# Performance work log

Measured on AMD Instinct MI355X. Metric: run time of the kernel, lower is better.

Reference implementation:

```python
import jax, jax.numpy as jnp
from jax import lax
import numpy as np

HIDDEN = 1024
FEAT = 512
PREV = 10
PRED = 20
BATCH = 1024


def setup_inputs() -> dict:
    key = jax.random.key(0)
    ks = jax.random.split(key, 12)
    s_in = 1.0 / np.sqrt(FEAT)
    s_h = 1.0 / np.sqrt(HIDDEN)
    return {
        "real_input": jax.random.normal(ks[0], (BATCH, PREV + PRED, FEAT), jnp.float32),
        "fake_input": jax.random.normal(ks[1], (BATCH, PRED, FEAT), jnp.float32),
        "Wx": jax.random.normal(ks[2], (FEAT, 4 * HIDDEN), jnp.float32) * s_in,
        "Wh": jax.random.normal(ks[3], (HIDDEN, 4 * HIDDEN), jnp.float32) * s_h,
        "b": jnp.zeros((4 * HIDDEN,), jnp.float32),
        "w2": jax.random.normal(ks[4], (HIDDEN, 1), jnp.float32) * s_h,
        "b2": jnp.zeros((1,), jnp.float32),
        "w3": jax.random.normal(ks[5], (1, 1), jnp.float32),
        "b3": jnp.zeros((1,), jnp.float32),
        "w4": jax.random.normal(ks[6], (1, 1), jnp.float32),
        "b4": jnp.zeros((1,), jnp.float32),
    }


def _lstm_hidden_states(seq, Wx, Wh, b):
    # seq: [B, T, F] -> hidden states hs: [T, B, H]
    B = seq.shape[0]
    xz = jnp.einsum("btf,fk->btk", seq, Wx) + b  # precompute input projections

    def step(carry, xz_t):
        h, c = carry
        z = xz_t + h @ Wh  # [B, 4H]
        i, f, g, o = jnp.split(z, 4, axis=-1)
        i = jax.nn.sigmoid(i)
        f = jax.nn.sigmoid(f)
        g = jnp.tanh(g)
        o = jax.nn.sigmoid(o)
        c = f * c + i * g
        h = o * jnp.tanh(c)
        return (h, c), h

    h0 = jnp.zeros((B, Wh.shape[0]), seq.dtype)
    _, hs = lax.scan(step, (h0, h0), jnp.swapaxes(xz, 0, 1))
    return hs


def _dense_chain(h, w2, b2, w3, b3, w4, b4):
    x = jnp.tanh(h @ w2 + b2)
    x = jnp.tanh(x @ w3 + b3)
    x = jnp.tanh(x @ w4 + b4)
    return x


def reference(real_input, fake_input, Wx, Wh, b, w2, b2, w3, b3, w4, b4):
    # trajectory_real[k] is the prefix real_input[:, :PREV+k+1]; running the
    # LSTM from zero state over each prefix equals taking hidden state at
    # step PREV+k of a single scan over the full sequence.
    fake_seq = jnp.concatenate([real_input[:, :PREV, :], fake_input], axis=1)

    hs_real = _lstm_hidden_states(real_input, Wx, Wh, b)[PREV:PREV + PRED]  # [PRED,B,H]
    hs_fake = _lstm_hidden_states(fake_seq, Wx, Wh, b)[PREV:PREV + PRED]

    real_pred = _dense_chain(hs_real, w2, b2, w3, b3, w4, b4)  # [PRED,B,1]
    fake_pred = _dense_chain(hs_fake, w2, b2, w3, b3, w4, b4)

    real_pred = jnp.swapaxes(real_pred, 0, 1)  # [B,PRED,1]
    fake_pred = jnp.swapaxes(fake_pred, 0, 1)
    return real_pred, fake_pred
```

## Files before the change

### kernel.cpp

```cpp
#include <hip/hip_runtime.h>
#include <hip/hip_bf16.h>
#include <stdint.h>
#include <string.h>

#define HIDDEN 1024
#define FEAT   512
#define PREV   10
#define PRED   20
#define BATCH  1024
#define KTOT   (HIDDEN + FEAT)
#define N4H    4096
#define TSTEPS (PREV + PRED)
#define NBLK   512
#define NTHR   512

typedef __attribute__((ext_vector_type(8))) short short8;
typedef __attribute__((ext_vector_type(4))) float f32x4;
typedef unsigned long long ull;

typedef __attribute__((address_space(3))) unsigned int u32_lds;
typedef const __attribute__((address_space(1))) unsigned int u32_gbl;

__device__ __forceinline__ void async16(void* lds, const void* g) {
  u32_lds* lp = (u32_lds*)(unsigned int)(uintptr_t)lds;
  u32_gbl* gp = (u32_gbl*)(uintptr_t)g;
  __builtin_amdgcn_global_load_lds(gp, lp, 16, 0, 0);
}

__device__ __forceinline__ float sigmoidf_(float x) {
  return 1.0f / (1.0f + __expf(-x));
}
__device__ __forceinline__ float tanhf_(float x) {
  return 1.0f - 2.0f / (1.0f + __expf(2.0f * x));
}

__device__ __forceinline__ ull cload(const void* p) {
  return __hip_atomic_load((const ull*)p, __ATOMIC_RELAXED, __HIP_MEMORY_SCOPE_AGENT);
}
__device__ __forceinline__ void cstore(void* p, ull v) {
  __hip_atomic_store((ull*)p, v, __ATOMIC_RELAXED, __HIP_MEMORY_SCOPE_AGENT);
}

__global__ void pack_w_kernel(const float* __restrict__ Wx, const float* __restrict__ Wh,
                              __hip_bfloat16* __restrict__ WpT) {
  __shared__ float tile[64][65];
  const int k0 = blockIdx.x * 64, n0 = blockIdx.y * 64;
  const int tid = threadIdx.x;
  const float* src = (k0 < HIDDEN) ? (Wh + (size_t)k0 * N4H) : (Wx + (size_t)(k0 - HIDDEN) * N4H);
  {
    const int jl = tid & 15, g = (tid >> 4) & 3, klb = tid >> 6;
#pragma unroll
    for (int it = 0; it < 16; ++it) {
      int kl = klb + it * 4;
      tile[kl][4 * jl + g] = src[(size_t)kl * N4H + g * HIDDEN + (n0 >> 2) + jl];
    }
  }
  __syncthreads();
  {
    const int kl = tid & 63, nlb = tid >> 6;
#pragma unroll
    for (int it = 0; it < 16; ++it) {
      int nl = nlb + it * 4;
      WpT[(size_t)(n0 + nl) * KTOT + k0 + kl] = __float2bfloat16(tile[kl][nl]);
    }
  }
}

__global__ void pack_bias_kernel(const float* __restrict__ b, float* __restrict__ bp) {
  int n = blockIdx.x * 256 + threadIdx.x;
  if (n < N4H) bp[n] = b[(n & 3) * HIDDEN + (n >> 2)];
}

__global__ void cvt_x_kernel(const float* __restrict__ xr, const float* __restrict__ xf,
                             __hip_bfloat16* __restrict__ xrb, __hip_bfloat16* __restrict__ xfb) {
  const int NR4 = BATCH * TSTEPS * FEAT / 4;
  const int NF4 = BATCH * PRED * FEAT / 4;
  int i = blockIdx.x * 256 + threadIdx.x;
  float4 v;
  __hip_bfloat16* dst;
  if (i < NR4) {
    v = ((const float4*)xr)[i];
    dst = xrb + (size_t)i * 4;
  } else {
    int j = i - NR4;
    if (j >= NF4) return;
    v = ((const float4*)xf)[j];
    dst = xfb + (size_t)j * 4;
  }
  dst[0] = __float2bfloat16(v.x);
  dst[1] = __float2bfloat16(v.y);
  dst[2] = __float2bfloat16(v.z);
  dst[3] = __float2bfloat16(v.w);
}

__global__ __launch_bounds__(512, 4)
void lstm_persistent(const __hip_bfloat16* __restrict__ xrb,
                     const __hip_bfloat16* __restrict__ xfb,
                     const __hip_bfloat16* __restrict__ WpT,
                     const float* __restrict__ biasp,
                     const float* __restrict__ w2,
                     __hip_bfloat16* __restrict__ hb0,
                     __hip_bfloat16* __restrict__ hb1,
                     float* __restrict__ cbuf,
                     float* __restrict__ accout,
                     unsigned* __restrict__ bar) {
  __shared__ __align__(16) char smem[40960];
  char* smA = smem;
  char* smB = smem + 8192;

  const int tid = threadIdx.x;
  const int bid = blockIdx.x;
  const int nt = bid & 15, rt = bid >> 4;
  const int n0 = nt * 256;
  const int r0 = rt * 64;
  const int w = tid >> 6, l = tid & 63;
  const int sub = l >> 3;
  const int csrc = (l & 7) ^ sub;
  const int quad = l >> 4, lrow = l & 15;
  const int wm = w & 1, wn = w >> 1;
  const int row_e = tid >> 3, jq = tid & 7;
  unsigned* cnt = bar;
  unsigned* flag = bar + 32;

  const unsigned short* wp_us = (const unsigned short*)WpT;
  float creg[8] = {0.f, 0.f, 0.f, 0.f, 0.f, 0.f, 0.f, 0.f};

#pragma unroll 1
  for (int t = 0; t < TSTEPS; ++t) {
    const unsigned short* hcur = (const unsigned short*)((t & 1) ? hb1 : hb0);
    unsigned short* hnext = (unsigned short*)((t & 1) ? hb0 : hb1);
    const bool active = (t >= PREV) || (rt < 16);

    if (active) {
      if (t == PREV && r0 >= BATCH) {
#pragma unroll
        for (int h2 = 0; h2 < 2; ++h2) {
          size_t base = (size_t)(r0 - BATCH + row_e) * HIDDEN + nt * 64 + h2 * 32 + jq * 4;
          ull d0 = cload(&cbuf[base]);
          ull d1 = cload(&cbuf[base + 2]);
          float2 f0 = *(float2*)&d0, f1 = *(float2*)&d1;
          creg[h2 * 4 + 0] = f0.x;
          creg[h2 * 4 + 1] = f0.y;
          creg[h2 * 4 + 2] = f1.x;
          creg[h2 * 4 + 3] = f1.y;
        }
      }
      const int r0h = (t == PREV && r0 >= BATCH) ? (r0 - BATCH) : r0;

      f32x4 acc[2][4];
#pragma unroll
      for (int a = 0; a < 2; ++a)
#pragma unroll
        for (int b_ = 0; b_ < 4; ++b_) acc[a][b_] = (f32x4){0.f, 0.f, 0.f, 0.f};

#pragma unroll 1
      for (int kt = 0; kt < KTOT / 64; ++kt) {
        const int k0 = kt * 64;
        const unsigned short* bb = wp_us + (size_t)n0 * KTOT + k0;
#pragma unroll
        for (int it = 0; it < 4; ++it)
          async16(smB + (w * 32 + it * 8) * 128,
                  bb + (size_t)(w * 32 + it * 8 + sub) * KTOT + csrc * 8);
        if (k0 < HIDDEN) {
          const unsigned short* ap = hcur + (size_t)(r0h + w * 8 + sub) * HIDDEN + k0 + csrc * 8;
          ull d0 = cload(ap);
          ull d1 = cload(ap + 4);
          ull* lw = (ull*)(smA + (w * 8 + sub) * 128 + (l & 7) * 16);
          lw[0] = d0;
          lw[1] = d1;
        } else {
          const unsigned short* xb;
          size_t xstr;
          if (r0 < BATCH) {
            xb = (const unsigned short*)xrb + ((size_t)r0 * TSTEPS + t) * FEAT + (k0 - HIDDEN);
            xstr = TSTEPS * FEAT;
          } else {
            xb = (const unsigned short*)xfb + ((size_t)(r0 - BATCH) * PRED + (t - PREV)) * FEAT + (k0 - HIDDEN);
            xstr = PRED * FEAT;
          }
          async16(smA + (w * 8) * 128, xb + (size_t)(w * 8 + sub) * xstr + csrc * 8);
        }
        __syncthreads();
#pragma unroll
        for (int kk = 0; kk < 2; ++kk) {
          const int swz = (((kk << 2) + quad) ^ (lrow & 7)) * 16;
          short8 af[2], bf[4];
#pragma unroll
          for (int mi = 0; mi < 2; ++mi)
            af[mi] = *(const short8*)(smA + (wm * 32 + mi * 16 + lrow) * 128 + swz);
#pragma unroll
          for (int ni = 0; ni < 4; ++ni)
            bf[ni] = *(const short8*)(smB + (wn * 64 + ni * 16 + lrow) * 128 + swz);
#pragma unroll
          for (int mi = 0; mi < 2; ++mi)
#pragma unroll
            for (int ni = 0; ni < 4; ++ni)
              acc[mi][ni] = __builtin_amdgcn_mfma_f32_16x16x32_bf16(af[mi], bf[ni], acc[mi][ni], 0, 0, 0);
        }
        __syncthreads();
      }

      float* zb = (float*)smem;
      const int kout = t - PREV;
#pragma unroll 1
      for (int h2 = 0; h2 < 2; ++h2) {
        if ((wn >> 1) == h2) {
          const int cb = (wn & 1) * 64;
#pragma unroll
          for (int mi = 0; mi < 2; ++mi)
#pragma unroll
            for (int ni = 0; ni < 4; ++ni) {
              f32x4 v = acc[mi][ni];
              int col = cb + ni * 16 + lrow;
              int rb = wm * 32 + mi * 16 + quad * 4;
#pragma unroll
              for (int r = 0; r < 4; ++r) zb[(rb + r) * 132 + col] = v[r];
            }
        }
        __syncthreads();
        unsigned short hs[4];
        float cn[4];
        float psum = 0.f;
#pragma unroll
        for (int it = 0; it < 4; ++it) {
          int jloc = jq * 4 + it;
          float4 z4 = *(float4*)&zb[row_e * 132 + jloc * 4];
          float4 bi = *(const float4*)&biasp[n0 + h2 * 128 + jloc * 4];
          int jg = nt * 64 + h2 * 32 + jloc;
          float gi = sigmoidf_(z4.x + bi.x);
          float gf = sigmoidf_(z4.y + bi.y);
          float gg = tanhf_(z4.z + bi.z);
          float go = sigmoidf_(z4.w + bi.w);
          int ci = h2 * 4 + it;
          float cnew = gf * creg[ci] + gi * gg;
          float hnew = go * tanhf_(cnew);
          creg[ci] = cnew;
          cn[it] = cnew;
          __hip_bfloat16 hbv = __float2bfloat16(hnew);
          hs[it] = *(unsigned short*)&hbv;
          if (t >= PREV) psum += hnew * w2[jg];
        }
        const int rg = r0 + row_e;
        const int jg0 = nt * 64 + h2 * 32 + jq * 4;
        ull hpack;
        memcpy(&hpack, hs, 8);
        cstore(&hnext[(size_t)rg * HIDDEN + jg0], hpack);
        if (t == PREV - 1) {
          ull c01, c23;
          memcpy(&c01, &cn[0], 8);
          memcpy(&c23, &cn[2], 8);
          cstore(&cbuf[(size_t)rg * HIDDEN + jg0], c01);
          cstore(&cbuf[(size_t)rg * HIDDEN + jg0 + 2], c23);
        }
        if (t >= PREV) {
          psum += __shfl_down(psum, 4, 8);
          psum += __shfl_down(psum, 2, 8);
          psum += __shfl_down(psum, 1, 8);
          if ((tid & 7) == 0) atomicAdd(&accout[rg * PRED + kout], psum);
        }
        __syncthreads();
      }
    }

    if (t < TSTEPS - 1) {
      __syncthreads();
      if (tid == 0) {
        unsigned ph = (unsigned)(t + 1);
        unsigned old = __hip_atomic_fetch_add(cnt, 1u, __ATOMIC_RELAXED, __HIP_MEMORY_SCOPE_AGENT);
        if (old == NBLK - 1) {
          __hip_atomic_store(cnt, 0u, __ATOMIC_RELAXED, __HIP_MEMORY_SCOPE_AGENT);
          __hip_atomic_store(flag, ph, __ATOMIC_RELAXED, __HIP_MEMORY_SCOPE_AGENT);
        } else {
          while (__hip_atomic_load(flag, __ATOMIC_RELAXED, __HIP_MEMORY_SCOPE_AGENT) < ph)
            __builtin_amdgcn_s_sleep(4);
        }
      }
      __syncthreads();
    }
  }
}

__global__ void final_kernel(const float* __restrict__ accout, const float* __restrict__ b2,
                             const float* __restrict__ w3, const float* __restrict__ b3,
                             const float* __restrict__ w4, const float* __restrict__ b4,
                             float* __restrict__ out) {
  int i = blockIdx.x * 256 + threadIdx.x;
  const int half = BATCH * PRED;
  if (i >= 2 * half) return;
  int r, k;
  if (i < half) {
    r = i / PRED;
    k = i % PRED;
  } else {
    r = BATCH + (i - half) / PRED;
    k = (i - half) % PRED;
  }
  float x = tanhf_(accout[r * PRED + k] + b2[0]);
  x = tanhf_(x * w3[0] + b3[0]);
  x = tanhf_(x * w4[0] + b4[0]);
  out[i] = x;
}

extern "C" void kernel_launch(void* const* d_in, const int* in_sizes, int n_in,
                              void* d_out, int out_size, void* d_ws, size_t ws_size,
                              hipStream_t stream) {
  const float* real_input = (const float*)d_in[0];
  const float* fake_input = (const float*)d_in[1];
  const float* Wx = (const float*)d_in[2];
  const float* Wh = (const float*)d_in[3];
  const float* b  = (const float*)d_in[4];
  const float* w2 = (const float*)d_in[5];
  const float* b2 = (const float*)d_in[6];
  const float* w3 = (const float*)d_in[7];
  const float* b3 = (const float*)d_in[8];
  const float* w4 = (const float*)d_in[9];
  const float* b4 = (const float*)d_in[10];
  float* out = (float*)d_out;

  char* ws = (char*)d_ws;
  size_t off = 0;
  __hip_bfloat16* WpT = (__hip_bfloat16*)(ws + off);  off += (size_t)N4H * KTOT * 2;
  float* biasp = (float*)(ws + off);                  off += (size_t)N4H * 4;
  __hip_bfloat16* xrb = (__hip_bfloat16*)(ws + off);  off += (size_t)BATCH * TSTEPS * FEAT * 2;
  __hip_bfloat16* xfb = (__hip_bfloat16*)(ws + off);  off += (size_t)BATCH * PRED * FEAT * 2;
  __hip_bfloat16* hb0 = (__hip_bfloat16*)(ws + off);  off += (size_t)2 * BATCH * HIDDEN * 2;
  __hip_bfloat16* hb1 = (__hip_bfloat16*)(ws + off);  off += (size_t)2 * BATCH * HIDDEN * 2;
  float* cbuf = (float*)(ws + off);                   off += (size_t)BATCH * HIDDEN * 4;
  float* accout = (float*)(ws + off);                 off += (size_t)2 * BATCH * PRED * 4;
  unsigned* bar = (unsigned*)(ws + off);              off += 256;

  hipMemsetAsync(hb0, 0, (size_t)2 * BATCH * HIDDEN * 2, stream);
  hipMemsetAsync(accout, 0, (size_t)2 * BATCH * PRED * 4, stream);
  hipMemsetAsync(bar, 0, 256, stream);

  pack_w_kernel<<<dim3(KTOT / 64, N4H / 64), 256, 0, stream>>>(Wx, Wh, WpT);
  pack_bias_kernel<<<N4H / 256, 256, 0, stream>>>(b, biasp);
  {
    int n4 = BATCH * TSTEPS * FEAT / 4 + BATCH * PRED * FEAT / 4;
    cvt_x_kernel<<<(n4 + 255) / 256, 256, 0, stream>>>(real_input, fake_input, xrb, xfb);
  }

  {
    const __hip_bfloat16* a_xrb = xrb;
    const __hip_bfloat16* a_xfb = xfb;
    const __hip_bfloat16* a_WpT = WpT;
    const float* a_biasp = biasp;
    const float* a_w2 = w2;
    __hip_bfloat16* a_hb0 = hb0;
    __hip_bfloat16* a_hb1 = hb1;
    float* a_cbuf = cbuf;
    float* a_acc = accout;
    unsigned* a_bar = bar;
    void* args[10] = {&a_xrb, &a_xfb, &a_WpT, &a_biasp, &a_w2,
                      &a_hb0, &a_hb1, &a_cbuf, &a_acc, &a_bar};
    hipError_t e = hipLaunchCooperativeKernel((const void*)lstm_persistent,
                                              dim3(NBLK), dim3(NTHR), args, 0, stream);
    if (e != hipSuccess) {
      lstm_persistent<<<dim3(NBLK), dim3(NTHR), 0, stream>>>(
          xrb, xfb, WpT, biasp, w2, hb0, hb1, cbuf, accout, bar);
    }
  }

  final_kernel<<<(2 * BATCH * PRED + 255) / 256, 256, 0, stream>>>(accout, b2, w3, b3, w4, b4, out);
}
```

Baseline: 1.342 ms.

## Double tile rows per block and add triple-buffered async K-loop pipeline

Each block now covers 128 batch rows instead of 64, so the persistent grid shrinks from 512 to 256 blocks and each B-weight tile loaded into LDS is reused across twice as many rows. The K loop becomes a three-stage software pipeline: weight and x tiles arrive through async global-to-LDS loads and h tiles through coherent dwordx4 loads, with explicit vmcnt waits so loads for step k+2 overlap the MFMAs for step k. The aim is to cut weight reloads and hide global latency inside each recurrent step, and fewer blocks also make the grid barrier cheaper. In exchange, shared memory per block rises to 144 KB and accumulator registers double, lowering occupancy, and the hand-written waitcnt sequence is fragile.

Measured after the change: 1.218 ms. 1.1x faster.

```diff
diff --git a/kernel.cpp b/kernel.cpp
--- a/kernel.cpp
+++ b/kernel.cpp
@@ -11,8 +11,10 @@
 #define KTOT   (HIDDEN + FEAT)
 #define N4H    4096
 #define TSTEPS (PREV + PRED)
-#define NBLK   512
+#define NBLK   256
 #define NTHR   512
+#define NKT    24
+#define BUFB   49152
 
 typedef __attribute__((ext_vector_type(8))) short short8;
 typedef __attribute__((ext_vector_type(4))) float f32x4;
@@ -39,6 +41,13 @@
 }
 __device__ __forceinline__ void cstore(void* p, ull v) {
   __hip_atomic_store((ull*)p, v, __ATOMIC_RELAXED, __HIP_MEMORY_SCOPE_AGENT);
+}
+
+__device__ __forceinline__ f32x4 cload16a(const void* p) {
+  f32x4 r;
+  asm volatile("global_load_dwordx4 %0, %1, off sc1"
+               : "=v"(r) : "v"(p) : "memory");
+  return r;
 }
 
 __global__ void pack_w_kernel(const float* __restrict__ Wx, const float* __restrict__ Wh,
@@ -93,7 +102,7 @@
   dst[3] = __float2bfloat16(v.w);
 }
 
-__global__ __launch_bounds__(512, 4)
+__global__ __launch_bounds__(512, 2)
 void lstm_persistent(const __hip_bfloat16* __restrict__ xrb,
                      const __hip_bfloat16* __restrict__ xfb,
                      const __hip_bfloat16* __restrict__ WpT,
@@ -104,166 +113,223 @@
                      float* __restrict__ cbuf,
                      float* __restrict__ accout,
                      unsigned* __restrict__ bar) {
-  __shared__ __align__(16) char smem[40960];
-  char* smA = smem;
-  char* smB = smem + 8192;
+  __shared__ __align__(16) char smem[3 * BUFB];
 
   const int tid = threadIdx.x;
   const int bid = blockIdx.x;
   const int nt = bid & 15, rt = bid >> 4;
   const int n0 = nt * 256;
-  const int r0 = rt * 64;
+  const int r0 = rt * 128;
   const int w = tid >> 6, l = tid & 63;
   const int sub = l >> 3;
   const int csrc = (l & 7) ^ sub;
   const int quad = l >> 4, lrow = l & 15;
-  const int wm = w & 1, wn = w >> 1;
-  const int row_e = tid >> 3, jq = tid & 7;
+  const int wm = w >> 2, wn = w & 3;
+  const int row_e = tid >> 2, jq = tid & 3;
   unsigned* cnt = bar;
   unsigned* flag = bar + 32;
 
   const unsigned short* wp_us = (const unsigned short*)WpT;
-  float creg[8] = {0.f, 0.f, 0.f, 0.f, 0.f, 0.f, 0.f, 0.f};
+  const unsigned short* bS = wp_us + (size_t)(n0 + w * 32 + sub) * KTOT + csrc * 8;
+  const int ldsAwr = (w * 16 + sub) * 128 + (l & 7) * 16;
+
+  float creg[16];
+#pragma unroll
+  for (int i = 0; i < 16; ++i) creg[i] = 0.f;
+
+#define ISSUE_STAGE(S, OFF, SA, SB)                                                   \
+  do {                                                                                \
+    const int _s = (S);                                                               \
+    char* _sb = smem + (OFF);                                                         \
+    async16(_sb + 16384 + (w * 32 + 0) * 128,  bS + (size_t)0 * 8 * KTOT + _s * 64);  \
+    async16(_sb + 16384 + (w * 32 + 8) * 128,  bS + (size_t)1 * 8 * KTOT + _s * 64);  \
+    async16(_sb + 16384 + (w * 32 + 16) * 128, bS + (size_t)2 * 8 * KTOT + _s * 64);  \
+    async16(_sb + 16384 + (w * 32 + 24) * 128, bS + (size_t)3 * 8 * KTOT + _s * 64);  \
+    if (_s < 16) {                                                                    \
+      SA = cload16a(hsA0 + (size_t)_s * 64);                                          \
+      SB = cload16a(hsA1 + (size_t)_s * 64);                                          \
+    } else {                                                                          \
+      async16(_sb + (w * 16) * 128,     xA0 + (size_t)(_s * 64 - HIDDEN));            \
+      async16(_sb + (w * 16 + 8) * 128, xA1 + (size_t)(_s * 64 - HIDDEN));            \
+    }                                                                                 \
+  } while (0)
+
+#define WRITE_A(OFFC, CA, CB)                                                         \
+  do {                                                                                \
+    *(f32x4*)(smem + (OFFC) + ldsAwr) = CA;                                           \
+    *(f32x4*)(smem + (OFFC) + ldsAwr + 1024) = CB;                                    \
+  } while (0)
+
+#define KT_COMPUTE(OFFC)                                                              \
+  do {                                                                                \
+    const char* _ca = smem + (OFFC);                                                  \
+    const char* _cb = _ca + 16384;                                                    \
+    _Pragma("unroll")                                                                 \
+    for (int kk = 0; kk < 2; ++kk) {                                                  \
+      const int swz = (((kk << 2) + quad) ^ (lrow & 7)) * 16;                         \
+      short8 af[4], bf[4];                                                            \
+      _Pragma("unroll")                                                               \
+      for (int mi = 0; mi < 4; ++mi)                                                  \
+        af[mi] = *(const short8*)(_ca + (wm * 64 + mi * 16 + lrow) * 128 + swz);      \
+      _Pragma("unroll")                                                               \
+      for (int ni = 0; ni < 4; ++ni)                                                  \
+        bf[ni] = *(const short8*)(_cb + (wn * 64 + ni * 16 + lrow) * 128 + swz);      \
+      _Pragma("unroll")                                                               \
+      for (int mi = 0; mi < 4; ++mi)                                                  \
+        _Pragma("unroll")                                                             \
+        for (int ni = 0; ni < 4; ++ni)                                                \
+          acc[mi][ni] = __builtin_amdgcn_mfma_f32_16x16x32_bf16(af[mi], bf[ni],       \
+                                                                acc[mi][ni], 0, 0, 0);\
+    }                                                                                 \
+  } while (0)
+
+#define KT_BODY(KT, OFFC, OFFS, CA, CB, SA, SB)                                       \
+  do {                                                                                \
+    if ((KT) < NKT - 2) ISSUE_STAGE((KT) + 2, OFFS, SA, SB);                          \
+    if ((KT) < NKT - 2) {                                                             \
+      asm volatile("s_waitcnt vmcnt(12)" ::: "memory");                               \
+    } else if ((KT) == NKT - 2) {                                                     \
+      asm volatile("s_waitcnt vmcnt(6)" ::: "memory");                                \
+    } else {                                                                          \
+      asm volatile("s_waitcnt vmcnt(0)" ::: "memory");                                \
+    }                                                                                 \
+    __builtin_amdgcn_sched_barrier(0);                                                \
+    if ((KT) < 16) {                                                                  \
+      WRITE_A(OFFC, CA, CB);                                                          \
+      asm volatile("s_waitcnt lgkmcnt(0)" ::: "memory");                              \
+      __builtin_amdgcn_sched_barrier(0);                                              \
+    }                                                                                 \
+    __builtin_amdgcn_s_barrier();                                                     \
+    __builtin_amdgcn_sched_barrier(0);                                                \
+    KT_COMPUTE(OFFC);                                                                 \
+    asm volatile("" ::: "memory");                                                    \
+    __builtin_amdgcn_s_barrier();                                                     \
+  } while (0)
 
 #pragma unroll 1
   for (int t = 0; t < TSTEPS; ++t) {
     const unsigned short* hcur = (const unsigned short*)((t & 1) ? hb1 : hb0);
-    unsigned short* hnext = (unsigned short*)((t & 1) ? hb0 : hb1);
-    const bool active = (t >= PREV) || (rt < 16);
+    unsigned short* hnx = (unsigned short*)((t & 1) ? hb0 : hb1);
+    const bool active = (t >= PREV) || (rt < 8);
 
     if (active) {
       if (t == PREV && r0 >= BATCH) {
 #pragma unroll
-        for (int h2 = 0; h2 < 2; ++h2) {
-          size_t base = (size_t)(r0 - BATCH + row_e) * HIDDEN + nt * 64 + h2 * 32 + jq * 4;
-          ull d0 = cload(&cbuf[base]);
-          ull d1 = cload(&cbuf[base + 2]);
-          float2 f0 = *(float2*)&d0, f1 = *(float2*)&d1;
-          creg[h2 * 4 + 0] = f0.x;
-          creg[h2 * 4 + 1] = f0.y;
-          creg[h2 * 4 + 2] = f1.x;
-          creg[h2 * 4 + 3] = f1.y;
-        }
+        for (int h2 = 0; h2 < 2; ++h2)
+#pragma unroll
+          for (int q = 0; q < 4; ++q) {
+            size_t base = (size_t)(r0 - BATCH + row_e) * HIDDEN + nt * 64 + h2 * 32 + jq * 8 + q * 2;
+            ull d = cload(&cbuf[base]);
+            float2 f = *(float2*)&d;
+            creg[h2 * 8 + q * 2 + 0] = f.x;
+            creg[h2 * 8 + q * 2 + 1] = f.y;
+          }
       }
       const int r0h = (t == PREV && r0 >= BATCH) ? (r0 - BATCH) : r0;
 
-      f32x4 acc[2][4];
-#pragma unroll
-      for (int a = 0; a < 2; ++a)
+      const unsigned short* hsA0 = hcur + (size_t)(r0h + w * 16 + sub) * HIDDEN + csrc * 8;
+      const unsigned short* hsA1 = hsA0 + 8 * HIDDEN;
+      const unsigned short* xb;
+      size_t xstr;
+      if (r0 < BATCH) {
+        xb = (const unsigned short*)xrb + ((size_t)r0 * TSTEPS + t) * FEAT;
+        xstr = (size_t)TSTEPS * FEAT;
+      } else {
+        xb = (const unsigned short*)xfb + ((size_t)(r0 - BATCH) * PRED + (t - PREV)) * FEAT;
+        xstr = (size_t)PRED * FEAT;
+      }
+      const unsigned short* xA0 = xb + (w * 16 + sub) * xstr + csrc * 8;
+      const unsigned short* xA1 = xA0 + 8 * xstr;
+
+      f32x4 acc[4][4];
+#pragma unroll
+      for (int a = 0; a < 4; ++a)
 #pragma unroll
         for (int b_ = 0; b_ < 4; ++b_) acc[a][b_] = (f32x4){0.f, 0.f, 0.f, 0.f};
 
+      f32x4 h0a, h0b, h1a, h1b, h2a, h2b;
+      ISSUE_STAGE(0, 0, h0a, h0b);
+      ISSUE_STAGE(1, BUFB, h1a, h1b);
+
 #pragma unroll 1
-      for (int kt = 0; kt < KTOT / 64; ++kt) {
-        const int k0 = kt * 64;
-        const unsigned short* bb = wp_us + (size_t)n0 * KTOT + k0;
-#pragma unroll
-        for (int it = 0; it < 4; ++it)
-          async16(smB + (w * 32 + it * 8) * 128,
-                  bb + (size_t)(w * 32 + it * 8 + sub) * KTOT + csrc * 8);
-        if (k0 < HIDDEN) {
-          const unsigned short* ap = hcur + (size_t)(r0h + w * 8 + sub) * HIDDEN + k0 + csrc * 8;
-          ull d0 = cload(ap);
-          ull d1 = cload(ap + 4);
-          ull* lw = (ull*)(smA + (w * 8 + sub) * 128 + (l & 7) * 16);
-          lw[0] = d0;
-          lw[1] = d1;
-        } else {
-          const unsigned short* xb;
-          size_t xstr;
-          if (r0 < BATCH) {
-            xb = (const unsigned short*)xrb + ((size_t)r0 * TSTEPS + t) * FEAT + (k0 - HIDDEN);
-            xstr = TSTEPS * FEAT;
-          } else {
-            xb = (const unsigned short*)xfb + ((size_t)(r0 - BATCH) * PRED + (t - PREV)) * FEAT + (k0 - HIDDEN);
-            xstr = PRED * FEAT;
-          }
-          async16(smA + (w * 8) * 128, xb + (size_t)(w * 8 + sub) * xstr + csrc * 8);
-        }
-        __syncthreads();
-#pragma unroll
-        for (int kk = 0; kk < 2; ++kk) {
-          const int swz = (((kk << 2) + quad) ^ (lrow & 7)) * 16;
-          short8 af[2], bf[4];
-#pragma unroll
-          for (int mi = 0; mi < 2; ++mi)
-            af[mi] = *(const short8*)(smA + (wm * 32 + mi * 16 + lrow) * 128 + swz);
-#pragma unroll
-          for (int ni = 0; ni < 4; ++ni)
-            bf[ni] = *(const short8*)(smB + (wn * 64 + ni * 16 + lrow) * 128 + swz);
-#pragma unroll
-          for (int mi = 0; mi < 2; ++mi)
-#pragma unroll
-            for (int ni = 0; ni < 4; ++ni)
-              acc[mi][ni] = __builtin_amdgcn_mfma_f32_16x16x32_bf16(af[mi], bf[ni], acc[mi][ni], 0, 0, 0);
-        }
-        __syncthreads();
+      for (int m = 0; m < 8; ++m) {
+        const int kt = 3 * m;
+        KT_BODY(kt + 0, 0,        2 * BUFB, h0a, h0b, h2a, h2b);
+        KT_BODY(kt + 1, BUFB,     0,        h1a, h1b, h0a, h0b);
+        KT_BODY(kt + 2, 2 * BUFB, BUFB,     h2a, h2b, h1a, h1b);
       }
 
       float* zb = (float*)smem;
       const int kout = t - PREV;
-#pragma unroll 1
+#pragma unroll
       for (int h2 = 0; h2 < 2; ++h2) {
         if ((wn >> 1) == h2) {
           const int cb = (wn & 1) * 64;
 #pragma unroll
-          for (int mi = 0; mi < 2; ++mi)
+          for (int mi = 0; mi < 4; ++mi)
 #pragma unroll
             for (int ni = 0; ni < 4; ++ni) {
               f32x4 v = acc[mi][ni];
               int col = cb + ni * 16 + lrow;
-              int rb = wm * 32 + mi * 16 + quad * 4;
+              int rb = wm * 64 + mi * 16 + quad * 4;
 #pragma unroll
               for (int r = 0; r < 4; ++r) zb[(rb + r) * 132 + col] = v[r];
             }
         }
         __syncthreads();
-        unsigned short hs[4];
-        float cn[4];
+        const int jg0 = nt * 64 + h2 * 32 + jq * 8;
+        const float4 w2a = *(const float4*)&w2[jg0];
+        const float4 w2b = *(const float4*)&w2[jg0 + 4];
+        float w2r[8] = {w2a.x, w2a.y, w2a.z, w2a.w, w2b.x, w2b.y, w2b.z, w2b.w};
+        unsigned short hsv[8];
+        float cnv[8];
         float psum = 0.f;
 #pragma unroll
-        for (int it = 0; it < 4; ++it) {
-          int jloc = jq * 4 + it;
+        for (int it = 0; it < 8; ++it) {
+          int jloc = jq * 8 + it;
           float4 z4 = *(float4*)&zb[row_e * 132 + jloc * 4];
           float4 bi = *(const float4*)&biasp[n0 + h2 * 128 + jloc * 4];
-          int jg = nt * 64 + h2 * 32 + jloc;
           float gi = sigmoidf_(z4.x + bi.x);
           float gf = sigmoidf_(z4.y + bi.y);
           float gg = tanhf_(z4.z + bi.z);
           float go = sigmoidf_(z4.w + bi.w);
-          int ci = h2 * 4 + it;
+          int ci = h2 * 8 + it;
           float cnew = gf * creg[ci] + gi * gg;
           float hnew = go * tanhf_(cnew);
           creg[ci] = cnew;
-          cn[it] = cnew;
+          cnv[it] = cnew;
           __hip_bfloat16 hbv = __float2bfloat16(hnew);
-          hs[it] = *(unsigned short*)&hbv;
-          if (t >= PREV) psum += hnew * w2[jg];
+          hsv[it] = *(unsigned short*)&hbv;
+          if (t >= PREV) psum += hnew * w2r[it];
         }
         const int rg = r0 + row_e;
-        const int jg0 = nt * 64 + h2 * 32 + jq * 4;
-        ull hpack;
-        memcpy(&hpack, hs, 8);
-        cstore(&hnext[(size_t)rg * HIDDEN + jg0], hpack);
+        {
+          ull p0, p1;
+          memcpy(&p0, &hsv[0], 8);
+          memcpy(&p1, &hsv[4], 8);
+          cstore(hnx + (size_t)rg * HIDDEN + jg0, p0);
+          cstore(hnx + (size_t)rg * HIDDEN + jg0 + 4, p1);
+        }
         if (t == PREV - 1) {
-          ull c01, c23;
-          memcpy(&c01, &cn[0], 8);
-          memcpy(&c23, &cn[2], 8);
-          cstore(&cbuf[(size_t)rg * HIDDEN + jg0], c01);
-          cstore(&cbuf[(size_t)rg * HIDDEN + jg0 + 2], c23);
+#pragma unroll
+          for (int q = 0; q < 4; ++q) {
+            ull d;
+            memcpy(&d, &cnv[2 * q], 8);
+            cstore(&cbuf[(size_t)rg * HIDDEN + jg0 + 2 * q], d);
+          }
         }
         if (t >= PREV) {
-          psum += __shfl_down(psum, 4, 8);
-          psum += __shfl_down(psum, 2, 8);
-          psum += __shfl_down(psum, 1, 8);
-          if ((tid & 7) == 0) atomicAdd(&accout[rg * PRED + kout], psum);
+          psum += __shfl_down(psum, 2, 4);
+          psum += __shfl_down(psum, 1, 4);
+          if (jq == 0) atomicAdd(&accout[rg * PRED + kout], psum);
         }
         __syncthreads();
       }
     }
 
     if (t < TSTEPS - 1) {
-      __syncthreads();
+      asm volatile("s_waitcnt vmcnt(0)" ::: "memory");
+      __builtin_amdgcn_s_barrier();
       if (tid == 0) {
         unsigned ph = (unsigned)(t + 1);
         unsigned old = __hip_atomic_fetch_add(cnt, 1u, __ATOMIC_RELAXED, __HIP_MEMORY_SCOPE_AGENT);
@@ -275,9 +341,13 @@
             __builtin_amdgcn_s_sleep(4);
         }
       }
-      __syncthreads();
+      __builtin_amdgcn_s_barrier();
     }
   }
+#undef ISSUE_STAGE
+#undef WRITE_A
+#undef KT_COMPUTE
+#undef KT_BODY
 }
 
 __global__ void final_kernel(const float* __restrict__ accout, const float* __restrict__ b2,
```

## Stream pre-fragmented weights into registers and double-buffer LDS in persistent LSTM

Applied to the files above, without the earlier changes.

Repacks the weight matrix into MFMA-fragment order so each wave loads its weight operands straight into registers, ping-ponging two register sets across k-tiles instead of staging weights through shared memory. Row tiles grow from 64 to 128 rows and the grid halves to 256 blocks, with a double-buffered LDS tile for h and x so the next tile loads while the current one computes. Gate math now runs directly on MFMA accumulators and stages h through a small transposed LDS tile for coalesced stores. Weight traffic per block and barrier count should drop, at the cost of higher register pressure (launch bounds lowered to 2 blocks per CU), fewer blocks, and extra pack work.

Result: slower. 1.401 ms (+4.4%).

```diff
diff --git a/kernel.cpp b/kernel.cpp
--- a/kernel.cpp
+++ b/kernel.cpp
@@ -11,8 +11,10 @@
 #define KTOT   (HIDDEN + FEAT)
 #define N4H    4096
 #define TSTEPS (PREV + PRED)
-#define NBLK   512
+#define NBLK   256
 #define NTHR   512
+#define NKT    24
+#define TILEB  16384
 
 typedef __attribute__((ext_vector_type(8))) short short8;
 typedef __attribute__((ext_vector_type(4))) float f32x4;
@@ -39,6 +41,12 @@
 }
 __device__ __forceinline__ void cstore(void* p, ull v) {
   __hip_atomic_store((ull*)p, v, __ATOMIC_RELAXED, __HIP_MEMORY_SCOPE_AGENT);
+}
+__device__ __forceinline__ float cload4(const void* p) {
+  return __hip_atomic_load((const float*)p, __ATOMIC_RELAXED, __HIP_MEMORY_SCOPE_AGENT);
+}
+__device__ __forceinline__ void cstore4(void* p, float v) {
+  __hip_atomic_store((float*)p, v, __ATOMIC_RELAXED, __HIP_MEMORY_SCOPE_AGENT);
 }
 
 __global__ void pack_w_kernel(const float* __restrict__ Wx, const float* __restrict__ Wh,
@@ -64,6 +72,17 @@
       WpT[(size_t)(n0 + nl) * KTOT + k0 + kl] = __float2bfloat16(tile[kl][nl]);
     }
   }
+}
+
+__global__ void pack_wf_kernel(const __hip_bfloat16* __restrict__ WpT,
+                               __hip_bfloat16* __restrict__ Wf) {
+  int id = blockIdx.x * 256 + threadIdx.x;
+  if (id >= (N4H / 16) * (KTOT / 32) * 64) return;
+  int l = id & 63, fg = id >> 6;
+  int kg = fg % (KTOT / 32), ng = fg / (KTOT / 32);
+  int n = ng * 16 + (l & 15);
+  int k0 = kg * 32 + (l >> 4) * 8;
+  *(short8*)(Wf + (size_t)id * 8) = *(const short8*)(WpT + (size_t)n * KTOT + k0);
 }
 
 __global__ void pack_bias_kernel(const float* __restrict__ b, float* __restrict__ bp) {
@@ -93,10 +112,10 @@
   dst[3] = __float2bfloat16(v.w);
 }
 
-__global__ __launch_bounds__(512, 4)
+__global__ __launch_bounds__(512, 2)
 void lstm_persistent(const __hip_bfloat16* __restrict__ xrb,
                      const __hip_bfloat16* __restrict__ xfb,
-                     const __hip_bfloat16* __restrict__ WpT,
+                     const __hip_bfloat16* __restrict__ Wf,
                      const float* __restrict__ biasp,
                      const float* __restrict__ w2,
                      __hip_bfloat16* __restrict__ hb0,
@@ -104,165 +123,203 @@
                      float* __restrict__ cbuf,
                      float* __restrict__ accout,
                      unsigned* __restrict__ bar) {
-  __shared__ __align__(16) char smem[40960];
-  char* smA = smem;
-  char* smB = smem + 8192;
+  __shared__ __align__(16) char smem[2 * TILEB + 128 * 68 * 2];
 
   const int tid = threadIdx.x;
   const int bid = blockIdx.x;
   const int nt = bid & 15, rt = bid >> 4;
   const int n0 = nt * 256;
-  const int r0 = rt * 64;
+  const int r0 = rt * 128;
   const int w = tid >> 6, l = tid & 63;
   const int sub = l >> 3;
   const int csrc = (l & 7) ^ sub;
   const int quad = l >> 4, lrow = l & 15;
-  const int wm = w & 1, wn = w >> 1;
-  const int row_e = tid >> 3, jq = tid & 7;
+  const int wn = w & 3, wb = w >> 2;
   unsigned* cnt = bar;
   unsigned* flag = bar + 32;
-
-  const unsigned short* wp_us = (const unsigned short*)WpT;
-  float creg[8] = {0.f, 0.f, 0.f, 0.f, 0.f, 0.f, 0.f, 0.f};
+  unsigned short* hT = (unsigned short*)(smem + 2 * TILEB);
+
+  const char* wfL = (const char*)Wf + ((size_t)(nt * 16 + wn * 4) * (KTOT / 32)) * 1024 + (size_t)l * 16;
+  const int ldsW = (w * 16 + sub) * 128 + (l & 7) * 16;
+
+  float w2r[4];
+#pragma unroll
+  for (int mi = 0; mi < 4; ++mi) w2r[mi] = w2[nt * 64 + wn * 16 + mi * 4 + quad];
+
+  float creg[16];
+#pragma unroll
+  for (int i = 0; i < 16; ++i) creg[i] = 0.f;
+
+  short8 wSA[8], wSB[8];
+  ull sd0, sd1, sd2, sd3;
+
+#define ISSUE_W(S, WS)                                                                 \
+  do {                                                                                 \
+    if ((S) < NKT) {                                                                   \
+      const char* _wp = wfL + (size_t)(S) * 2048;                                      \
+      _Pragma("unroll")                                                                \
+      for (int _mi = 0; _mi < 4; ++_mi)                                                \
+        _Pragma("unroll")                                                              \
+        for (int _kk = 0; _kk < 2; ++_kk)                                              \
+          WS[_mi * 2 + _kk] =                                                          \
+              *(const short8*)(_wp + _mi * ((KTOT / 32) * 1024) + _kk * 1024);         \
+    }                                                                                  \
+  } while (0)
+
+#define STAGE_ISSUE(S)                                                                 \
+  do {                                                                                 \
+    if ((S) < 16) {                                                                    \
+      sd0 = cload(hsA0 + (size_t)(S) * 64);                                            \
+      sd1 = cload(hsA0 + (size_t)(S) * 64 + 4);                                        \
+      sd2 = cload(hsA1 + (size_t)(S) * 64);                                            \
+      sd3 = cload(hsA1 + (size_t)(S) * 64 + 4);                                        \
+    } else if ((S) < NKT) {                                                            \
+      char* _sb = smem + ((S) & 1) * TILEB;                                            \
+      async16(_sb + (w * 16) * 128,     xA0 + (size_t)((S) * 64 - HIDDEN));            \
+      async16(_sb + (w * 16 + 8) * 128, xA1 + (size_t)((S) * 64 - HIDDEN));            \
+    }                                                                                  \
+  } while (0)
+
+#define STAGE_WRITE(S)                                                                 \
+  do {                                                                                 \
+    if ((S) < 16) {                                                                    \
+      ull* _lw = (ull*)(smem + ((S) & 1) * TILEB + ldsW);                              \
+      _lw[0] = sd0;                                                                    \
+      _lw[1] = sd1;                                                                    \
+      ull* _lw2 = (ull*)(smem + ((S) & 1) * TILEB + ldsW + 1024);                      \
+      _lw2[0] = sd2;                                                                   \
+      _lw2[1] = sd3;                                                                   \
+    }                                                                                  \
+  } while (0)
+
+#define KT_COMPUTE(KT, WS)                                                             \
+  do {                                                                                 \
+    const char* _cb = smem + ((KT) & 1) * TILEB;                                       \
+    _Pragma("unroll")                                                                  \
+    for (int kk = 0; kk < 2; ++kk) {                                                   \
+      const int swz = (((kk << 2) + quad) ^ (lrow & 7)) * 16;                          \
+      short8 bf[4];                                                                    \
+      _Pragma("unroll")                                                                \
+      for (int bi = 0; bi < 4; ++bi)                                                   \
+        bf[bi] = *(const short8*)(_cb + (wb * 64 + bi * 16 + lrow) * 128 + swz);       \
+      _Pragma("unroll")                                                                \
+      for (int mi = 0; mi < 4; ++mi)                                                   \
+        _Pragma("unroll")                                                              \
+        for (int bi = 0; bi < 4; ++bi)                                                 \
+          acc[mi][bi] = __builtin_amdgcn_mfma_f32_16x16x32_bf16(WS[mi * 2 + kk],       \
+                            bf[bi], acc[mi][bi], 0, 0, 0);                             \
+    }                                                                                  \
+  } while (0)
+
+#define KT_BODY(KT, WSc, WSn)                                                          \
+  do {                                                                                 \
+    STAGE_ISSUE((KT) + 1);                                                             \
+    ISSUE_W((KT) + 1, WSn);                                                            \
+    KT_COMPUTE(KT, WSc);                                                               \
+    STAGE_WRITE((KT) + 1);                                                             \
+    __syncthreads();                                                                   \
+  } while (0)
 
 #pragma unroll 1
   for (int t = 0; t < TSTEPS; ++t) {
     const unsigned short* hcur = (const unsigned short*)((t & 1) ? hb1 : hb0);
-    unsigned short* hnext = (unsigned short*)((t & 1) ? hb0 : hb1);
-    const bool active = (t >= PREV) || (rt < 16);
+    unsigned short* hnx = (unsigned short*)((t & 1) ? hb0 : hb1);
+    const bool active = (t >= PREV) || (rt < 8);
 
     if (active) {
       if (t == PREV && r0 >= BATCH) {
 #pragma unroll
-        for (int h2 = 0; h2 < 2; ++h2) {
-          size_t base = (size_t)(r0 - BATCH + row_e) * HIDDEN + nt * 64 + h2 * 32 + jq * 4;
-          ull d0 = cload(&cbuf[base]);
-          ull d1 = cload(&cbuf[base + 2]);
-          float2 f0 = *(float2*)&d0, f1 = *(float2*)&d1;
-          creg[h2 * 4 + 0] = f0.x;
-          creg[h2 * 4 + 1] = f0.y;
-          creg[h2 * 4 + 2] = f1.x;
-          creg[h2 * 4 + 3] = f1.y;
-        }
+        for (int mi = 0; mi < 4; ++mi)
+#pragma unroll
+          for (int bi = 0; bi < 4; ++bi)
+            creg[mi * 4 + bi] = cload4(&cbuf[(size_t)(r0 - BATCH + wb * 64 + bi * 16 + lrow) * HIDDEN
+                                             + nt * 64 + wn * 16 + mi * 4 + quad]);
       }
       const int r0h = (t == PREV && r0 >= BATCH) ? (r0 - BATCH) : r0;
 
-      f32x4 acc[2][4];
-#pragma unroll
-      for (int a = 0; a < 2; ++a)
+      const unsigned short* hsA0 = hcur + (size_t)(r0h + w * 16 + sub) * HIDDEN + csrc * 8;
+      const unsigned short* hsA1 = hsA0 + 8 * HIDDEN;
+      const unsigned short* xb;
+      size_t xstr;
+      if (r0 < BATCH) {
+        xb = (const unsigned short*)xrb + ((size_t)r0 * TSTEPS + t) * FEAT;
+        xstr = (size_t)TSTEPS * FEAT;
+      } else {
+        xb = (const unsigned short*)xfb + ((size_t)(r0 - BATCH) * PRED + (t - PREV)) * FEAT;
+        xstr = (size_t)PRED * FEAT;
+      }
+      const unsigned short* xA0 = xb + (w * 16 + sub) * xstr + csrc * 8;
+      const unsigned short* xA1 = xA0 + 8 * xstr;
+
+      f32x4 acc[4][4];
+#pragma unroll
+      for (int a = 0; a < 4; ++a)
 #pragma unroll
         for (int b_ = 0; b_ < 4; ++b_) acc[a][b_] = (f32x4){0.f, 0.f, 0.f, 0.f};
 
+      STAGE_ISSUE(0);
+      if (t == 0) ISSUE_W(0, wSA);
+      STAGE_WRITE(0);
+      __syncthreads();
+
 #pragma unroll 1
-      for (int kt = 0; kt < KTOT / 64; ++kt) {
-        const int k0 = kt * 64;
-        const unsigned short* bb = wp_us + (size_t)n0 * KTOT + k0;
-#pragma unroll
-        for (int it = 0; it < 4; ++it)
-          async16(smB + (w * 32 + it * 8) * 128,
-                  bb + (size_t)(w * 32 + it * 8 + sub) * KTOT + csrc * 8);
-        if (k0 < HIDDEN) {
-          const unsigned short* ap = hcur + (size_t)(r0h + w * 8 + sub) * HIDDEN + k0 + csrc * 8;
-          ull d0 = cload(ap);
-          ull d1 = cload(ap + 4);
-          ull* lw = (ull*)(smA + (w * 8 + sub) * 128 + (l & 7) * 16);
-          lw[0] = d0;
-          lw[1] = d1;
-        } else {
-          const unsigned short* xb;
-          size_t xstr;
-          if (r0 < BATCH) {
-            xb = (const unsigned short*)xrb + ((size_t)r0 * TSTEPS + t) * FEAT + (k0 - HIDDEN);
-            xstr = TSTEPS * FEAT;
-          } else {
-            xb = (const unsigned short*)xfb + ((size_t)(r0 - BATCH) * PRED + (t - PREV)) * FEAT + (k0 - HIDDEN);
-            xstr = PRED * FEAT;
-          }
-          async16(smA + (w * 8) * 128, xb + (size_t)(w * 8 + sub) * xstr + csrc * 8);
-        }
-        __syncthreads();
-#pragma unroll
-        for (int kk = 0; kk < 2; ++kk) {
-          const int swz = (((kk << 2) + quad) ^ (lrow & 7)) * 16;
-          short8 af[2], bf[4];
-#pragma unroll
-          for (int mi = 0; mi < 2; ++mi)
-            af[mi] = *(const short8*)(smA + (wm * 32 + mi * 16 + lrow) * 128 + swz);
-#pragma unroll
-          for (int ni = 0; ni < 4; ++ni)
-            bf[ni] = *(const short8*)(smB + (wn * 64 + ni * 16 + lrow) * 128 + swz);
-#pragma unroll
-          for (int mi = 0; mi < 2; ++mi)
-#pragma unroll
-            for (int ni = 0; ni < 4; ++ni)
-              acc[mi][ni] = __builtin_amdgcn_mfma_f32_16x16x32_bf16(af[mi], bf[ni], acc[mi][ni], 0, 0, 0);
-        }
-        __syncthreads();
-      }
-
-      float* zb = (float*)smem;
+      for (int m2 = 0; m2 < NKT / 2; ++m2) {
+        const int kt = 2 * m2;
+        KT_BODY(kt, wSA, wSB);
+        KT_BODY(kt + 1, wSB, wSA);
+      }
+
       const int kout = t - PREV;
-#pragma unroll 1
-      for (int h2 = 0; h2 < 2; ++h2) {
-        if ((wn >> 1) == h2) {
-          const int cb = (wn & 1) * 64;
-#pragma unroll
-          for (int mi = 0; mi < 2; ++mi)
-#pragma unroll
-            for (int ni = 0; ni < 4; ++ni) {
-              f32x4 v = acc[mi][ni];
-              int col = cb + ni * 16 + lrow;
-              int rb = wm * 32 + mi * 16 + quad * 4;
-#pragma unroll
-              for (int r = 0; r < 4; ++r) zb[(rb + r) * 132 + col] = v[r];
-            }
-        }
-        __syncthreads();
-        unsigned short hs[4];
-        float cn[4];
-        float psum = 0.f;
-#pragma unroll
-        for (int it = 0; it < 4; ++it) {
-          int jloc = jq * 4 + it;
-          float4 z4 = *(float4*)&zb[row_e * 132 + jloc * 4];
-          float4 bi = *(const float4*)&biasp[n0 + h2 * 128 + jloc * 4];
-          int jg = nt * 64 + h2 * 32 + jloc;
-          float gi = sigmoidf_(z4.x + bi.x);
-          float gf = sigmoidf_(z4.y + bi.y);
-          float gg = tanhf_(z4.z + bi.z);
-          float go = sigmoidf_(z4.w + bi.w);
-          int ci = h2 * 4 + it;
+      float psum[4] = {0.f, 0.f, 0.f, 0.f};
+#pragma unroll
+      for (int mi = 0; mi < 4; ++mi) {
+        const float4 bi4 = *(const float4*)&biasp[n0 + wn * 64 + mi * 16 + quad * 4];
+#pragma unroll
+        for (int bi = 0; bi < 4; ++bi) {
+          f32x4 z = acc[mi][bi];
+          float gi = sigmoidf_(z[0] + bi4.x);
+          float gf = sigmoidf_(z[1] + bi4.y);
+          float gg = tanhf_(z[2] + bi4.z);
+          float go = sigmoidf_(z[3] + bi4.w);
+          const int ci = mi * 4 + bi;
           float cnew = gf * creg[ci] + gi * gg;
           float hnew = go * tanhf_(cnew);
           creg[ci] = cnew;
-          cn[it] = cnew;
           __hip_bfloat16 hbv = __float2bfloat16(hnew);
-          hs[it] = *(unsigned short*)&hbv;
-          if (t >= PREV) psum += hnew * w2[jg];
+          hT[(wb * 64 + bi * 16 + lrow) * 68 + wn * 16 + mi * 4 + quad] =
+              *(unsigned short*)&hbv;
+          if (t >= PREV) psum[bi] += hnew * w2r[mi];
+          if (t == PREV - 1)
+            cstore4(&cbuf[(size_t)(r0 + wb * 64 + bi * 16 + lrow) * HIDDEN
+                          + nt * 64 + wn * 16 + mi * 4 + quad], cnew);
         }
-        const int rg = r0 + row_e;
-        const int jg0 = nt * 64 + h2 * 32 + jq * 4;
-        ull hpack;
-        memcpy(&hpack, hs, 8);
-        cstore(&hnext[(size_t)rg * HIDDEN + jg0], hpack);
-        if (t == PREV - 1) {
-          ull c01, c23;
-          memcpy(&c01, &cn[0], 8);
-          memcpy(&c23, &cn[2], 8);
-          cstore(&cbuf[(size_t)rg * HIDDEN + jg0], c01);
-          cstore(&cbuf[(size_t)rg * HIDDEN + jg0 + 2], c23);
+      }
+      __syncthreads();
+      {
+        const int er = tid >> 2, ejq = tid & 3;
+#pragma unroll
+        for (int it = 0; it < 4; ++it) {
+          int jl = ejq * 16 + it * 4;
+          ull v;
+          memcpy(&v, &hT[er * 68 + jl], 8);
+          cstore(hnx + (size_t)(r0 + er) * HIDDEN + nt * 64 + jl, v);
         }
-        if (t >= PREV) {
-          psum += __shfl_down(psum, 4, 8);
-          psum += __shfl_down(psum, 2, 8);
-          psum += __shfl_down(psum, 1, 8);
-          if ((tid & 7) == 0) atomicAdd(&accout[rg * PRED + kout], psum);
+      }
+      if (t >= PREV) {
+#pragma unroll
+        for (int bi = 0; bi < 4; ++bi) {
+          float v = psum[bi];
+          v += __shfl_down(v, 32);
+          v += __shfl_down(v, 16);
+          if (quad == 0)
+            atomicAdd(&accout[(size_t)(r0 + wb * 64 + bi * 16 + lrow) * PRED + kout], v);
         }
-        __syncthreads();
       }
     }
 
     if (t < TSTEPS - 1) {
+      const bool nact = (t + 1 >= PREV) || (rt < 8);
+      if (nact) ISSUE_W(0, wSA);
       __syncthreads();
       if (tid == 0) {
         unsigned ph = (unsigned)(t + 1);
@@ -278,6 +335,11 @@
       __syncthreads();
     }
   }
+#undef ISSUE_W
+#undef STAGE_ISSUE
+#undef STAGE_WRITE
+#undef KT_COMPUTE
+#undef KT_BODY
 }
 
 __global__ void final_kernel(const float* __restrict__ accout, const float* __restrict__ b2,
@@ -319,15 +381,16 @@
 
   char* ws = (char*)d_ws;
   size_t off = 0;
-  __hip_bfloat16* WpT = (__hip_bfloat16*)(ws + off);  off += (size_t)N4H * KTOT * 2;
+  __hip_bfloat16* Wf = (__hip_bfloat16*)(ws + off);   off += (size_t)N4H * KTOT * 2;
   float* biasp = (float*)(ws + off);                  off += (size_t)N4H * 4;
-  __hip_bfloat16* xrb = (__hip_bfloat16*)(ws + off);  off += (size_t)BATCH * TSTEPS * FEAT * 2;
-  __hip_bfloat16* xfb = (__hip_bfloat16*)(ws + off);  off += (size_t)BATCH * PRED * FEAT * 2;
   __hip_bfloat16* hb0 = (__hip_bfloat16*)(ws + off);  off += (size_t)2 * BATCH * HIDDEN * 2;
   __hip_bfloat16* hb1 = (__hip_bfloat16*)(ws + off);  off += (size_t)2 * BATCH * HIDDEN * 2;
   float* cbuf = (float*)(ws + off);                   off += (size_t)BATCH * HIDDEN * 4;
   float* accout = (float*)(ws + off);                 off += (size_t)2 * BATCH * PRED * 4;
   unsigned* bar = (unsigned*)(ws + off);              off += 256;
+  __hip_bfloat16* xrb = (__hip_bfloat16*)(ws + off);
+  __hip_bfloat16* WpT = (__hip_bfloat16*)(ws + off);  off += (size_t)BATCH * TSTEPS * FEAT * 2;
+  __hip_bfloat16* xfb = (__hip_bfloat16*)(ws + off);  off += (size_t)BATCH * PRED * FEAT * 2;
 
   hipMemsetAsync(hb0, 0, (size_t)2 * BATCH * HIDDEN * 2, stream);
   hipMemsetAsync(accout, 0, (size_t)2 * BATCH * PRED * 4, stream);
@@ -335,6 +398,7 @@
 
   pack_w_kernel<<<dim3(KTOT / 64, N4H / 64), 256, 0, stream>>>(Wx, Wh, WpT);
   pack_bias_kernel<<<N4H / 256, 256, 0, stream>>>(b, biasp);
+  pack_wf_kernel<<<((N4H / 16) * (KTOT / 32) * 64 + 255) / 256, 256, 0, stream>>>(WpT, Wf);
   {
     int n4 = BATCH * TSTEPS * FEAT / 4 + BATCH * PRED * FEAT / 4;
     cvt_x_kernel<<<(n4 + 255) / 256, 256, 0, stream>>>(real_input, fake_input, xrb, xfb);
@@ -343,7 +407,7 @@
   {
     const __hip_bfloat16* a_xrb = xrb;
     const __hip_bfloat16* a_xfb = xfb;
-    const __hip_bfloat16* a_WpT = WpT;
+    const __hip_bfloat16* a_Wf = Wf;
     const float* a_biasp = biasp;
     const float* a_w2 = w2;
     __hip_bfloat16* a_hb0 = hb0;
@@ -351,13 +415,13 @@
     float* a_cbuf = cbuf;
     float* a_acc = accout;
     unsigned* a_bar = bar;
-    void* args[10] = {&a_xrb, &a_xfb, &a_WpT, &a_biasp, &a_w2,
+    void* args[10] = {&a_xrb, &a_xfb, &a_Wf, &a_biasp, &a_w2,
                       &a_hb0, &a_hb1, &a_cbuf, &a_acc, &a_bar};
     hipError_t e = hipLaunchCooperativeKernel((const void*)lstm_persistent,
                                               dim3(NBLK), dim3(NTHR), args, 0, stream);
     if (e != hipSuccess) {
       lstm_persistent<<<dim3(NBLK), dim3(NTHR), 0, stream>>>(
-          xrb, xfb, WpT, biasp, w2, hb0, hb1, cbuf, accout, bar);
+          xrb, xfb, Wf, biasp, w2, hb0, hb1, cbuf, accout, bar);
     }
   }
 
```
